# Optimization experiments

Hardware: AMD Instinct MI355X
Metric: run time of the kernel (lower is better)

## Reference

```python
import jax, jax.numpy as jnp
import numpy as np

NUM_USERS = 100000
NUM_ITEMS = 50000
EMB_DIM = 64
NUM_LAYERS = 3
N_EDGES = 3200000
BATCH = 16384


def setup_inputs() -> dict:
    key = jax.random.key(0)
    ks = jax.random.split(key, 6)
    user_emb = jax.random.normal(ks[0], (NUM_USERS, EMB_DIM), dtype=jnp.float32) * 0.1
    item_emb = jax.random.normal(ks[1], (NUM_ITEMS, EMB_DIM), dtype=jnp.float32) * 0.1
    # normalized adjacency values ~ 1/degree scale to keep propagation stable
    edge_vals = jax.random.uniform(ks[2], (N_EDGES,), dtype=jnp.float32) * (1.0 / 32.0)
    edge_u = jax.random.randint(ks[3], (N_EDGES,), 0, NUM_USERS, dtype=jnp.int32)
    edge_i = jax.random.randint(ks[4], (N_EDGES,), 0, NUM_ITEMS, dtype=jnp.int32)
    ku, ki = jax.random.split(ks[5])
    users = jax.random.randint(ku, (BATCH,), 0, NUM_USERS, dtype=jnp.int32)
    items = jax.random.randint(ki, (BATCH,), 0, NUM_ITEMS, dtype=jnp.int32)
    return {
        "user_emb": user_emb, "item_emb": item_emb, "edge_vals": edge_vals,
        "edge_u": edge_u, "edge_i": edge_i, "users": users, "items": items,
    }


def reference(user_emb, item_emb, edge_vals, edge_u, edge_i, users, items):
    num_users, num_items = user_emb.shape[0], item_emb.shape[0]
    e_u, e_i = user_emb, item_emb
    sum_u, sum_i = user_emb, item_emb
    for _ in range(NUM_LAYERS):
        # e_i^{k+1} = M_ui @ e_u^{k}  (SpMM: gather user rows, scatter-add to items)
        new_i = jax.ops.segment_sum(edge_vals[:, None] * e_u[edge_u], edge_i,
                                    num_segments=num_items)
        # e_u^{k+1} = M_iu @ e_i^{k}  (transpose SpMM)
        new_u = jax.ops.segment_sum(edge_vals[:, None] * e_i[edge_i], edge_u,
                                    num_segments=num_users)
        e_u, e_i = new_u, new_i
        sum_u = sum_u + e_u
        sum_i = sum_i + e_i
    inv = 1.0 / (NUM_LAYERS + 1)
    eu_f = sum_u * inv  # Eq (3.25): layer-mean
    ei_f = sum_i * inv
    # Eq (3.26): y_hat(u,i) = e_u^T e_i
    return (eu_f[users] * ei_f[items]).sum(axis=1)
```

## Files before the change

### kernel.cpp

```cpp
#include <hip/hip_runtime.h>
#include <stdint.h>

#define D 64
#define SH_I 8
#define SH_U 9
#define EPT 8
#define TILE 4096
#define PAD 8
#define SRT_CAP 18944

typedef unsigned long long u64;
typedef unsigned int u32;

#define DUMMY64 0xFFFFFFFF00000000ull


__device__ __forceinline__ u32 bf16_rne(float f) {
    u32 x = __float_as_uint(f);
    return (x + 0x7fffu + ((x >> 16) & 1u)) >> 16;
}
__device__ __forceinline__ u32 pack2_bf16(float a, float b) {
    return bf16_rne(a) | (bf16_rne(b) << 16);
}

__global__ __launch_bounds__(256)
void cvt_bf16_kernel(const float2* __restrict__ src, u32* __restrict__ dst, long n2) {
    long i = (long)blockIdx.x * blockDim.x + threadIdx.x;
    long stride = (long)gridDim.x * blockDim.x;
    for (; i < n2; i += stride) {
        float2 f = src[i];
        dst[i] = pack2_bf16(f.x, f.y);
    }
}


__device__ __forceinline__ int excl_scan_512t(int v, int* wsum) {
    int tid = threadIdx.x, lane = tid & 63, wid = tid >> 6;
    int x = v;
    #pragma unroll
    for (int d = 1; d < 64; d <<= 1) { int t = __shfl_up(x, d, 64); if (lane >= d) x += t; }
    if (lane == 63) wsum[wid] = x;
    __syncthreads();
    if (tid < 8) {
        int y = wsum[tid];
        #pragma unroll
        for (int d = 1; d < 8; d <<= 1) { int t = __shfl_up(y, d, 8); if (tid >= d) y += t; }
        wsum[tid] = y;
    }
    __syncthreads();
    return ((wid > 0) ? wsum[wid - 1] : 0) + x - v;
}

__device__ __forceinline__ int excl_scan_1024t(int v, int* wsum16) {
    int tid = threadIdx.x, lane = tid & 63, wid = tid >> 6;
    int x = v;
    #pragma unroll
    for (int d = 1; d < 64; d <<= 1) { int t = __shfl_up(x, d, 64); if (lane >= d) x += t; }
    if (lane == 63) wsum16[wid] = x;
    __syncthreads();
    if (tid < 16) {
        int y = wsum16[tid];
        #pragma unroll
        for (int d = 1; d < 16; d <<= 1) { int t = __shfl_up(y, d, 16); if (tid >= d) y += t; }
        wsum16[tid] = y;
    }
    __syncthreads();
    return ((wid > 0) ? wsum16[wid - 1] : 0) + x - v;
}


__global__ __launch_bounds__(512)
void init_cursors_kernel(int* cur_i, int* rc_i, int nb_i, int cap_i,
                         int* cur_u, int* rc_u, int nb_u, int cap_u) {
    int t = threadIdx.x;
    if (t < nb_i) { cur_i[t] = t * cap_i; rc_i[t] = 0; }
    if (t < nb_u) { cur_u[t] = t * cap_u; rc_u[t] = 0; }
}

__global__ __launch_bounds__(512)
void passA_kernel(const int* __restrict__ eu, const int* __restrict__ ei,
                  const float* __restrict__ ev, int E,
                  int* __restrict__ cur_i, int* __restrict__ rc_i,
                  int* __restrict__ cur_u, int* __restrict__ rc_u,
                  u64* __restrict__ stg_i, u64* __restrict__ stg_u) {
    __shared__ u64 stage[TILE];
    __shared__ int cnt[256], loffs[256], gbase[256];
    __shared__ int wsum[8];
    int tid = threadIdx.x;
    long tile0 = (long)blockIdx.x * TILE;
    int uu[EPT], ii[EPT], lo[EPT];
    u32 vv[EPT];
    #pragma unroll
    for (int j = 0; j < EPT; ++j) {
        long e = tile0 + tid + j * 512;
        if (e < E) {
            uu[j] = eu[e]; ii[j] = ei[e];
            vv[j] = bf16_rne(ev[e]) & 0x7fffu;
        } else {
            uu[j] = -1;
        }
    }

    if (tid < 256) cnt[tid] = 0;
    __syncthreads();
    #pragma unroll
    for (int j = 0; j < EPT; ++j)
        if (uu[j] >= 0) lo[j] = atomicAdd(&cnt[ii[j] >> SH_I], 1);
    __syncthreads();
    {
        int c = (tid < 256) ? cnt[tid] : 0;
        int excl = excl_scan_512t(c, wsum);
        if (tid < 256) {
            loffs[tid] = excl;
            if (c) {
                int cp = (c + PAD - 1) & ~(PAD - 1);
                gbase[tid] = atomicAdd(&cur_i[tid], cp);
                atomicAdd(&rc_i[tid], c);
            }
        }
    }
    __syncthreads();
    #pragma unroll
    for (int j = 0; j < EPT; ++j) {
        if (uu[j] >= 0) {
            int b = ii[j] >> SH_I;
            u32 rec = (vv[j] << 17) | (u32)uu[j];
            stage[loffs[b] + lo[j]] =
                ((u64)(u32)(ii[j] & ((1 << SH_I) - 1)) << 32) | rec;
        }
    }
    __syncthreads();
    {
        int w = tid >> 6, lane = tid & 63;
        for (int b = w; b < 256; b += 8) {
            int c = cnt[b];
            if (!c) continue;
            int cp = (c + PAD - 1) & ~(PAD - 1);
            int lb = loffs[b];
            long gb = gbase[b];
            for (int r = lane; r < cp; r += 64)
                stg_i[gb + r] = (r < c) ? stage[lb + r] : DUMMY64;
        }
    }
    __syncthreads();

    if (tid < 256) cnt[tid] = 0;
    __syncthreads();
    #pragma unroll
    for (int j = 0; j < EPT; ++j)
        if (uu[j] >= 0) lo[j] = atomicAdd(&cnt[uu[j] >> SH_U], 1);
    __syncthreads();
    {
        int c = (tid < 256) ? cnt[tid] : 0;
        int excl = excl_scan_512t(c, wsum);
        if (tid < 256) {
            loffs[tid] = excl;
            if (c) {
                int cp = (c + PAD - 1) & ~(PAD - 1);
                gbase[tid] = atomicAdd(&cur_u[tid], cp);
                atomicAdd(&rc_u[tid], c);
            }
        }
    }
    __syncthreads();
    #pragma unroll
    for (int j = 0; j < EPT; ++j) {
        if (uu[j] >= 0) {
            int b = uu[j] >> SH_U;
            u32 rec = (vv[j] << 17) | (u32)ii[j];
            stage[loffs[b] + lo[j]] =
                ((u64)(u32)(uu[j] & ((1 << SH_U) - 1)) << 32) | rec;
        }
    }
    __syncthreads();
    {
        int w = tid >> 6, lane = tid & 63;
        for (int b = w; b < 256; b += 8) {
            int c = cnt[b];
            if (!c) continue;
            int cp = (c + PAD - 1) & ~(PAD - 1);
            int lb = loffs[b];
            long gb = gbase[b];
            for (int r = lane; r < cp; r += 64)
                stg_u[gb + r] = (r < c) ? stage[lb + r] : DUMMY64;
        }
    }
}

__global__ __launch_bounds__(512)
void bucket_scan_kernel(const int* __restrict__ rc, int nb, int E,
                        int* __restrict__ bbase, int* __restrict__ rowp_sentinel) {
    __shared__ int wsum[8];
    int tid = threadIdx.x;
    int v = (tid < nb) ? rc[tid] : 0;
    int excl = excl_scan_512t(v, wsum);
    if (tid < nb) bbase[tid] = excl;
    if (tid == 0) *rowp_sentinel = E;
}

__global__ __launch_bounds__(1024)
void passB_kernel(int nb_i, int cap_i, int N_i,
                  int nb_u, int cap_u, int N_u,
                  const int* __restrict__ cur_i, const int* __restrict__ cur_u,
                  const int* __restrict__ rc_i, const int* __restrict__ rc_u,
                  const int* __restrict__ bb_i, const int* __restrict__ bb_u,
                  const u64* __restrict__ stg_i, const u64* __restrict__ stg_u,
                  int* __restrict__ rowp_i, int* __restrict__ rowp_u,
                  u32* __restrict__ csr_i, u32* __restrict__ csr_u) {
    __shared__ u32 srt[SRT_CAP];
    __shared__ int lcnt[512];
    __shared__ int wsum[16];
    int b = blockIdx.x;
    int dir_item = (b < nb_i);
    int bb = dir_item ? b : b - nb_i;
    int SH = dir_item ? SH_I : SH_U;
    int cap = dir_item ? cap_i : cap_u;
    int N = dir_item ? N_i : N_u;
    const u64* stg = dir_item ? stg_i : stg_u;
    int ebase = dir_item ? bb_i[bb] : bb_u[bb];
    int scount = (dir_item ? cur_i[bb] : cur_u[bb]) - bb * cap;
    int realcnt = dir_item ? rc_i[bb] : rc_u[bb];
    int* rowp = dir_item ? rowp_i : rowp_u;
    u32* csr = dir_item ? csr_i : csr_u;

    int rows0 = bb << SH;
    int nrows = min(1 << SH, N - rows0);
    int tid = threadIdx.x;
    const uint4* stg4 = (const uint4*)(stg + (size_t)bb * cap);
    int npair = scount >> 1;

    if (tid < 512) lcnt[tid] = 0;
    __syncthreads();
    for (int k = tid; k < npair; k += 1024) {
        uint4 w = stg4[k];
        if ((int)w.y >= 0) atomicAdd(&lcnt[(int)w.y], 1);
        if ((int)w.w >= 0) atomicAdd(&lcnt[(int)w.w], 1);
    }
    __syncthreads();
    int v = (tid < 512) ? lcnt[tid] : 0;
    int excl = excl_scan_1024t(v, wsum);
    if (tid < 512) lcnt[tid] = excl;
    if (tid < nrows) rowp[rows0 + tid] = ebase + excl;
    __syncthreads();
    for (int k = tid; k < npair; k += 1024) {
        uint4 w = stg4[k];
        if ((int)w.y >= 0) {
            int p = atomicAdd(&lcnt[(int)w.y], 1);
            if (p < SRT_CAP) srt[p] = w.x;
        }
        if ((int)w.w >= 0) {
            int p = atomicAdd(&lcnt[(int)w.w], 1);
            if (p < SRT_CAP) srt[p] = w.z;
        }
    }
    __syncthreads();
    int n = min(realcnt, SRT_CAP);
    for (int k = tid; k < n; k += 1024)
        csr[ebase + k] = srt[k];
}


template<int SAMPLED>
__global__ __launch_bounds__(256)
void spmm_kernel(const int* __restrict__ rowptr, const u32* __restrict__ csr,
                 const u32* __restrict__ src16, u32* __restrict__ dst16,
                 const int* __restrict__ idx, int nrows) {
    int slot = blockIdx.x * 4 + (threadIdx.x >> 6);
    if (slot >= nrows) return;
    int row = SAMPLED ? idx[slot] : slot;
    int lane = threadIdx.x & 63;
    int g = lane >> 4;
    int el = lane & 15;
    int beg = rowptr[row], end = rowptr[row + 1];
    const uint2* SB = (const uint2*)src16 + el;
    float4 A0 = {0,0,0,0}, A1 = {0,0,0,0}, A2 = {0,0,0,0}, A3 = {0,0,0,0};
    for (int k = beg + g; k < end; k += 16) {
        u32 r0 = csr[k];
        u32 r1 = csr[k + 4];
        u32 r2 = csr[k + 8];
        u32 r3 = csr[k + 12];
        bool m1 = (k + 4) < end, m2 = (k + 8) < end, m3 = (k + 12) < end;
        int s0 = (int)(r0 & 0x1ffffu);
        int s1 = m1 ? (int)(r1 & 0x1ffffu) : 0;
        int s2 = m2 ? (int)(r2 & 0x1ffffu) : 0;
        int s3 = m3 ? (int)(r3 & 0x1ffffu) : 0;
        float v0 = __uint_as_float((r0 & 0xfffe0000u) >> 1);
        float v1 = m1 ? __uint_as_float((r1 & 0xfffe0000u) >> 1) : 0.f;
        float v2 = m2 ? __uint_as_float((r2 & 0xfffe0000u) >> 1) : 0.f;
        float v3 = m3 ? __uint_as_float((r3 & 0xfffe0000u) >> 1) : 0.f;
        uint2 w0 = SB[(size_t)s0 * 16];
        uint2 w1 = SB[(size_t)s1 * 16];
        uint2 w2 = SB[(size_t)s2 * 16];
        uint2 w3 = SB[(size_t)s3 * 16];
        A0.x += v0 * __uint_as_float(w0.x << 16);
        A0.y += v0 * __uint_as_float(w0.x & 0xffff0000u);
        A0.z += v0 * __uint_as_float(w0.y << 16);
        A0.w += v0 * __uint_as_float(w0.y & 0xffff0000u);
        A1.x += v1 * __uint_as_float(w1.x << 16);
        A1.y += v1 * __uint_as_float(w1.x & 0xffff0000u);
        A1.z += v1 * __uint_as_float(w1.y << 16);
        A1.w += v1 * __uint_as_float(w1.y & 0xffff0000u);
        A2.x += v2 * __uint_as_float(w2.x << 16);
        A2.y += v2 * __uint_as_float(w2.x & 0xffff0000u);
        A2.z += v2 * __uint_as_float(w2.y << 16);
        A2.w += v2 * __uint_as_float(w2.y & 0xffff0000u);
        A3.x += v3 * __uint_as_float(w3.x << 16);
        A3.y += v3 * __uint_as_float(w3.x & 0xffff0000u);
        A3.z += v3 * __uint_as_float(w3.y << 16);
        A3.w += v3 * __uint_as_float(w3.y & 0xffff0000u);
    }
    float4 a;
    a.x = (A0.x + A1.x) + (A2.x + A3.x);
    a.y = (A0.y + A1.y) + (A2.y + A3.y);
    a.z = (A0.z + A1.z) + (A2.z + A3.z);
    a.w = (A0.w + A1.w) + (A2.w + A3.w);
    a.x += __shfl_xor(a.x, 16, 64); a.x += __shfl_xor(a.x, 32, 64);
    a.y += __shfl_xor(a.y, 16, 64); a.y += __shfl_xor(a.y, 32, 64);
    a.z += __shfl_xor(a.z, 16, 64); a.z += __shfl_xor(a.z, 32, 64);
    a.w += __shfl_xor(a.w, 16, 64); a.w += __shfl_xor(a.w, 32, 64);
    if (g == 0) {
        ((uint2*)dst16)[(size_t)slot * 16 + el] =
            make_uint2(pack2_bf16(a.x, a.y), pack2_bf16(a.z, a.w));
    }
}

__global__ __launch_bounds__(256)
void score_kernel(const float* __restrict__ user_emb, const float* __restrict__ item_emb,
                  const u32* __restrict__ eu1, const u32* __restrict__ eu2,
                  const u32* __restrict__ eu3s,
                  const u32* __restrict__ ei1, const u32* __restrict__ ei2,
                  const u32* __restrict__ ei3s,
                  const int* __restrict__ users, const int* __restrict__ items,
                  float* __restrict__ out, int B, float inv2) {
    int gid = blockIdx.x * blockDim.x + threadIdx.x;
    int b = gid >> 4;
    int lane = gid & 15;
    if (b >= B) return;
    int u = users[b], it = items[b];

    float4 su = ((const float4*)(user_emb + (size_t)u * D))[lane];
    uint2 p1 = ((const uint2*)eu1)[(size_t)u * 16 + lane];
    uint2 p2 = ((const uint2*)eu2)[(size_t)u * 16 + lane];
    uint2 p3 = ((const uint2*)eu3s)[(size_t)b * 16 + lane];
    su.x += __uint_as_float(p1.x << 16) + __uint_as_float(p2.x << 16) + __uint_as_float(p3.x << 16);
    su.y += __uint_as_float(p1.x & 0xffff0000u) + __uint_as_float(p2.x & 0xffff0000u) + __uint_as_float(p3.x & 0xffff0000u);
    su.z += __uint_as_float(p1.y << 16) + __uint_as_float(p2.y << 16) + __uint_as_float(p3.y << 16);
    su.w += __uint_as_float(p1.y & 0xffff0000u) + __uint_as_float(p2.y & 0xffff0000u) + __uint_as_float(p3.y & 0xffff0000u);

    float4 si = ((const float4*)(item_emb + (size_t)it * D))[lane];
    uint2 q1 = ((const uint2*)ei1)[(size_t)it * 16 + lane];
    uint2 q2 = ((const uint2*)ei2)[(size_t)it * 16 + lane];
    uint2 q3 = ((const uint2*)ei3s)[(size_t)b * 16 + lane];
    si.x += __uint_as_float(q1.x << 16) + __uint_as_float(q2.x << 16) + __uint_as_float(q3.x << 16);
    si.y += __uint_as_float(q1.x & 0xffff0000u) + __uint_as_float(q2.x & 0xffff0000u) + __uint_as_float(q3.x & 0xffff0000u);
    si.z += __uint_as_float(q1.y << 16) + __uint_as_float(q2.y << 16) + __uint_as_float(q3.y << 16);
    si.w += __uint_as_float(q1.y & 0xffff0000u) + __uint_as_float(q2.y & 0xffff0000u) + __uint_as_float(q3.y & 0xffff0000u);

    float d = su.x * si.x + su.y * si.y + su.z * si.z + su.w * si.w;
    #pragma unroll
    for (int m = 1; m < 16; m <<= 1) d += __shfl_xor(d, m, 64);
    if (lane == 0) out[b] = d * inv2;
}


extern "C" void kernel_launch(void* const* d_in, const int* in_sizes, int n_in,
                              void* d_out, int out_size, void* d_ws, size_t ws_size,
                              hipStream_t stream) {
    const float* user_emb = (const float*)d_in[0];
    const float* item_emb = (const float*)d_in[1];
    const float* edge_vals = (const float*)d_in[2];
    const int* edge_u = (const int*)d_in[3];
    const int* edge_i = (const int*)d_in[4];
    const int* users = (const int*)d_in[5];
    const int* items = (const int*)d_in[6];
    float* out = (float*)d_out;

    const int U = in_sizes[0] / D;
    const int I = in_sizes[1] / D;
    const int E = in_sizes[2];
    const int B = in_sizes[5];

    const int nb_i = (I + (1 << SH_I) - 1) >> SH_I;
    const int nb_u = (U + (1 << SH_U) - 1) >> SH_U;
    const int tiles = (E + TILE - 1) / TILE;
    const int cap_i = ((E / nb_i + tiles * (PAD - 1) + 1024 + 63) / 64) * 64;
    const int cap_u = ((E / nb_u + tiles * (PAD - 1) + 1024 + 63) / 64) * 64;

    char* p = (char*)d_ws;
    size_t off = 0;
    auto alloc = [&](size_t bytes) -> char* {
        char* r = p + off;
        off = (off + bytes + 255) & ~(size_t)255;
        return r;
    };
    u32* ub16  = (u32*)alloc((size_t)U * (D / 2) * 4);
    u32* ib16  = (u32*)alloc((size_t)I * (D / 2) * 4);
    u32* eu1   = (u32*)alloc((size_t)U * (D / 2) * 4);
    u32* eu2   = (u32*)alloc((size_t)U * (D / 2) * 4);
    u32* ei1   = (u32*)alloc((size_t)I * (D / 2) * 4);
    u32* ei2   = (u32*)alloc((size_t)I * (D / 2) * 4);
    u32* eu3s  = (u32*)alloc((size_t)B * (D / 2) * 4);
    u32* ei3s  = (u32*)alloc((size_t)B * (D / 2) * 4);
    u32* csr_u = (u32*)alloc((size_t)(E + 16) * 4);
    u32* csr_i = (u32*)alloc((size_t)(E + 16) * 4);
    int* rowp_u = (int*)alloc((size_t)(U + 1) * 4);
    int* rowp_i = (int*)alloc((size_t)(I + 1) * 4);
    int* cur_i  = (int*)alloc((size_t)nb_i * 4);
    int* cur_u  = (int*)alloc((size_t)nb_u * 4);
    int* rc_i   = (int*)alloc((size_t)nb_i * 4);
    int* rc_u   = (int*)alloc((size_t)nb_u * 4);
    int* bb_i   = (int*)alloc((size_t)nb_i * 4);
    int* bb_u   = (int*)alloc((size_t)nb_u * 4);
    u64* stg_i  = (u64*)alloc((size_t)nb_i * cap_i * 8);
    u64* stg_u  = (u64*)alloc((size_t)nb_u * cap_u * 8);
    if (off > ws_size) return;

    cvt_bf16_kernel<<<1024, 256, 0, stream>>>((const float2*)user_emb, ub16, (long)U * (D / 2));
    cvt_bf16_kernel<<<1024, 256, 0, stream>>>((const float2*)item_emb, ib16, (long)I * (D / 2));

    init_cursors_kernel<<<1, 512, 0, stream>>>(cur_i, rc_i, nb_i, cap_i,
                                               cur_u, rc_u, nb_u, cap_u);
    passA_kernel<<<tiles, 512, 0, stream>>>(edge_u, edge_i, edge_vals, E,
                                            cur_i, rc_i, cur_u, rc_u,
                                            stg_i, stg_u);
    bucket_scan_kernel<<<1, 512, 0, stream>>>(rc_i, nb_i, E, bb_i, rowp_i + I);
    bucket_scan_kernel<<<1, 512, 0, stream>>>(rc_u, nb_u, E, bb_u, rowp_u + U);
    passB_kernel<<<nb_i + nb_u, 1024, 0, stream>>>(nb_i, cap_i, I, nb_u, cap_u, U,
                                                   cur_i, cur_u, rc_i, rc_u,
                                                   bb_i, bb_u,
                                                   stg_i, stg_u, rowp_i, rowp_u,
                                                   csr_i, csr_u);

    int blk_i = (I + 3) / 4;
    int blk_u = (U + 3) / 4;
    int blk_s = (B + 3) / 4;
    spmm_kernel<0><<<blk_i, 256, 0, stream>>>(rowp_i, csr_i, ub16, ei1, nullptr, I);
    spmm_kernel<0><<<blk_u, 256, 0, stream>>>(rowp_u, csr_u, ib16, eu1, nullptr, U);
    spmm_kernel<0><<<blk_i, 256, 0, stream>>>(rowp_i, csr_i, eu1, ei2, nullptr, I);
    spmm_kernel<0><<<blk_u, 256, 0, stream>>>(rowp_u, csr_u, ei1, eu2, nullptr, U);
    spmm_kernel<1><<<blk_s, 256, 0, stream>>>(rowp_i, csr_i, eu2, ei3s, items, B);
    spmm_kernel<1><<<blk_s, 256, 0, stream>>>(rowp_u, csr_u, ei2, eu3s, users, B);

    int blk_sc = (B * 16 + 255) / 256;
    score_kernel<<<blk_sc, 256, 0, stream>>>(user_emb, item_emb,
                                             eu1, eu2, eu3s, ei1, ei2, ei3s,
                                             users, items, out, B, 0.0625f);
}
```

Measured before the change: 321.7 us.

## Split bf16 embeddings into two column planes and run SpMM per half

```diff
diff --git a/kernel.cpp b/kernel.cpp
--- a/kernel.cpp
+++ b/kernel.cpp
@@ -24,12 +24,15 @@
 }
 
 __global__ __launch_bounds__(256)
-void cvt_bf16_kernel(const float2* __restrict__ src, u32* __restrict__ dst, long n2) {
+void cvt_bf16_kernel(const float2* __restrict__ src, u32* __restrict__ dst, int N) {
+    long n = (long)N * 32;
     long i = (long)blockIdx.x * blockDim.x + threadIdx.x;
     long stride = (long)gridDim.x * blockDim.x;
-    for (; i < n2; i += stride) {
+    for (; i < n; i += stride) {
         float2 f = src[i];
-        dst[i] = pack2_bf16(f.x, f.y);
+        long row = i >> 5;
+        int c = (int)(i & 31);
+        dst[(size_t)(c >> 4) * N * 16 + row * 16 + (c & 15)] = pack2_bf16(f.x, f.y);
     }
 }
 
@@ -132,13 +135,14 @@
     __syncthreads();
     {
         int w = tid >> 6, lane = tid & 63;
-        for (int b = w; b < 256; b += 8) {
+        int sub = lane >> 4, l16 = lane & 15;
+        for (int b = w * 4 + sub; b < 256; b += 32) {
             int c = cnt[b];
             if (!c) continue;
             int cp = (c + PAD - 1) & ~(PAD - 1);
             int lb = loffs[b];
             long gb = gbase[b];
-            for (int r = lane; r < cp; r += 64)
+            for (int r = l16; r < cp; r += 16)
                 stg_i[gb + r] = (r < c) ? stage[lb + r] : DUMMY64;
         }
     }
@@ -175,13 +179,14 @@
     __syncthreads();
     {
         int w = tid >> 6, lane = tid & 63;
-        for (int b = w; b < 256; b += 8) {
+        int sub = lane >> 4, l16 = lane & 15;
+        for (int b = w * 4 + sub; b < 256; b += 32) {
             int c = cnt[b];
             if (!c) continue;
             int cp = (c + PAD - 1) & ~(PAD - 1);
             int lb = loffs[b];
             long gb = gbase[b];
-            for (int r = lane; r < cp; r += 64)
+            for (int r = l16; r < cp; r += 16)
                 stg_u[gb + r] = (r < c) ? stage[lb + r] : DUMMY64;
         }
     }
@@ -260,19 +265,66 @@
 }
 
 
-template<int SAMPLED>
 __global__ __launch_bounds__(256)
-void spmm_kernel(const int* __restrict__ rowptr, const u32* __restrict__ csr,
-                 const u32* __restrict__ src16, u32* __restrict__ dst16,
-                 const int* __restrict__ idx, int nrows) {
+void spmm_half_kernel(const int* __restrict__ rowptr, const u32* __restrict__ csr,
+                      const u32* __restrict__ srcp, u32* __restrict__ dstp,
+                      int nrows) {
+    int row = blockIdx.x * 4 + (threadIdx.x >> 6);
+    if (row >= nrows) return;
+    int lane = threadIdx.x & 63;
+    int g = lane >> 3;
+    int el = lane & 7;
+    int beg = rowptr[row], end = rowptr[row + 1];
+    const uint2* SB = (const uint2*)srcp + el;
+    float4 A0 = {0,0,0,0}, A1 = {0,0,0,0};
+    for (int k = beg + g; k < end; k += 16) {
+        u32 r0 = __builtin_nontemporal_load(csr + k);
+        u32 r1 = __builtin_nontemporal_load(csr + k + 8);
+        bool m1 = (k + 8) < end;
+        int s0 = (int)(r0 & 0x1ffffu);
+        int s1 = m1 ? (int)(r1 & 0x1ffffu) : 0;
+        float v0 = __uint_as_float((r0 & 0xfffe0000u) >> 1);
+        float v1 = m1 ? __uint_as_float((r1 & 0xfffe0000u) >> 1) : 0.f;
+        uint2 w0 = SB[(size_t)s0 * 8];
+        uint2 w1 = SB[(size_t)s1 * 8];
+        A0.x += v0 * __uint_as_float(w0.x << 16);
+        A0.y += v0 * __uint_as_float(w0.x & 0xffff0000u);
+        A0.z += v0 * __uint_as_float(w0.y << 16);
+        A0.w += v0 * __uint_as_float(w0.y & 0xffff0000u);
+        A1.x += v1 * __uint_as_float(w1.x << 16);
+        A1.y += v1 * __uint_as_float(w1.x & 0xffff0000u);
+        A1.z += v1 * __uint_as_float(w1.y << 16);
+        A1.w += v1 * __uint_as_float(w1.y & 0xffff0000u);
+    }
+    float4 a;
+    a.x = A0.x + A1.x; a.y = A0.y + A1.y; a.z = A0.z + A1.z; a.w = A0.w + A1.w;
+    #pragma unroll
+    for (int m = 8; m < 64; m <<= 1) {
+        a.x += __shfl_xor(a.x, m, 64);
+        a.y += __shfl_xor(a.y, m, 64);
+        a.z += __shfl_xor(a.z, m, 64);
+        a.w += __shfl_xor(a.w, m, 64);
+    }
+    if (g == 0) {
+        u64 o = (u64)pack2_bf16(a.x, a.y) | ((u64)pack2_bf16(a.z, a.w) << 32);
+        __builtin_nontemporal_store(o, (u64*)dstp + (size_t)row * 8 + el);
+    }
+}
+
+__global__ __launch_bounds__(256)
+void spmm_sampled_kernel(const int* __restrict__ rowptr, const u32* __restrict__ csr,
+                         const u32* __restrict__ src_base, int splaneN,
+                         u32* __restrict__ dst16, const int* __restrict__ idx,
+                         int nrows) {
     int slot = blockIdx.x * 4 + (threadIdx.x >> 6);
     if (slot >= nrows) return;
-    int row = SAMPLED ? idx[slot] : slot;
+    int row = idx[slot];
     int lane = threadIdx.x & 63;
     int g = lane >> 4;
     int el = lane & 15;
     int beg = rowptr[row], end = rowptr[row + 1];
-    const uint2* SB = (const uint2*)src16 + el;
+    const uint2* SB = (const uint2*)(src_base + (size_t)(el >> 3) * splaneN * 16)
+                      + (el & 7);
     float4 A0 = {0,0,0,0}, A1 = {0,0,0,0}, A2 = {0,0,0,0}, A3 = {0,0,0,0};
     for (int k = beg + g; k < end; k += 16) {
         u32 r0 = csr[k];
@@ -288,10 +340,10 @@
         float v1 = m1 ? __uint_as_float((r1 & 0xfffe0000u) >> 1) : 0.f;
         float v2 = m2 ? __uint_as_float((r2 & 0xfffe0000u) >> 1) : 0.f;
         float v3 = m3 ? __uint_as_float((r3 & 0xfffe0000u) >> 1) : 0.f;
-        uint2 w0 = SB[(size_t)s0 * 16];
-        uint2 w1 = SB[(size_t)s1 * 16];
-        uint2 w2 = SB[(size_t)s2 * 16];
-        uint2 w3 = SB[(size_t)s3 * 16];
+        uint2 w0 = SB[(size_t)s0 * 8];
+        uint2 w1 = SB[(size_t)s1 * 8];
+        uint2 w2 = SB[(size_t)s2 * 8];
+        uint2 w3 = SB[(size_t)s3 * 8];
         A0.x += v0 * __uint_as_float(w0.x << 16);
         A0.y += v0 * __uint_as_float(w0.x & 0xffff0000u);
         A0.z += v0 * __uint_as_float(w0.y << 16);
@@ -331,16 +383,19 @@
                   const u32* __restrict__ ei1, const u32* __restrict__ ei2,
                   const u32* __restrict__ ei3s,
                   const int* __restrict__ users, const int* __restrict__ items,
-                  float* __restrict__ out, int B, float inv2) {
+                  float* __restrict__ out, int B, int U, int I, float inv2) {
     int gid = blockIdx.x * blockDim.x + threadIdx.x;
     int b = gid >> 4;
     int lane = gid & 15;
     if (b >= B) return;
     int u = users[b], it = items[b];
+    size_t upoff = (size_t)(lane >> 3) * U * 16;
+    size_t ipoff = (size_t)(lane >> 3) * I * 16;
+    int col = lane & 7;
 
     float4 su = ((const float4*)(user_emb + (size_t)u * D))[lane];
-    uint2 p1 = ((const uint2*)eu1)[(size_t)u * 16 + lane];
-    uint2 p2 = ((const uint2*)eu2)[(size_t)u * 16 + lane];
+    uint2 p1 = ((const uint2*)(eu1 + upoff))[(size_t)u * 8 + col];
+    uint2 p2 = ((const uint2*)(eu2 + upoff))[(size_t)u * 8 + col];
     uint2 p3 = ((const uint2*)eu3s)[(size_t)b * 16 + lane];
     su.x += __uint_as_float(p1.x << 16) + __uint_as_float(p2.x << 16) + __uint_as_float(p3.x << 16);
     su.y += __uint_as_float(p1.x & 0xffff0000u) + __uint_as_float(p2.x & 0xffff0000u) + __uint_as_float(p3.x & 0xffff0000u);
@@ -348,8 +403,8 @@
     su.w += __uint_as_float(p1.y & 0xffff0000u) + __uint_as_float(p2.y & 0xffff0000u) + __uint_as_float(p3.y & 0xffff0000u);
 
     float4 si = ((const float4*)(item_emb + (size_t)it * D))[lane];
-    uint2 q1 = ((const uint2*)ei1)[(size_t)it * 16 + lane];
-    uint2 q2 = ((const uint2*)ei2)[(size_t)it * 16 + lane];
+    uint2 q1 = ((const uint2*)(ei1 + ipoff))[(size_t)it * 8 + col];
+    uint2 q2 = ((const uint2*)(ei2 + ipoff))[(size_t)it * 8 + col];
     uint2 q3 = ((const uint2*)ei3s)[(size_t)b * 16 + lane];
     si.x += __uint_as_float(q1.x << 16) + __uint_as_float(q2.x << 16) + __uint_as_float(q3.x << 16);
     si.y += __uint_as_float(q1.x & 0xffff0000u) + __uint_as_float(q2.x & 0xffff0000u) + __uint_as_float(q3.x & 0xffff0000u);
@@ -415,8 +470,8 @@
     u64* stg_u  = (u64*)alloc((size_t)nb_u * cap_u * 8);
     if (off > ws_size) return;
 
-    cvt_bf16_kernel<<<1024, 256, 0, stream>>>((const float2*)user_emb, ub16, (long)U * (D / 2));
-    cvt_bf16_kernel<<<1024, 256, 0, stream>>>((const float2*)item_emb, ib16, (long)I * (D / 2));
+    cvt_bf16_kernel<<<1024, 256, 0, stream>>>((const float2*)user_emb, ub16, U);
+    cvt_bf16_kernel<<<1024, 256, 0, stream>>>((const float2*)item_emb, ib16, I);
 
     init_cursors_kernel<<<1, 512, 0, stream>>>(cur_i, rc_i, nb_i, cap_i,
                                                cur_u, rc_u, nb_u, cap_u);
@@ -434,15 +489,20 @@
     int blk_i = (I + 3) / 4;
     int blk_u = (U + 3) / 4;
     int blk_s = (B + 3) / 4;
-    spmm_kernel<0><<<blk_i, 256, 0, stream>>>(rowp_i, csr_i, ub16, ei1, nullptr, I);
-    spmm_kernel<0><<<blk_u, 256, 0, stream>>>(rowp_u, csr_u, ib16, eu1, nullptr, U);
-    spmm_kernel<0><<<blk_i, 256, 0, stream>>>(rowp_i, csr_i, eu1, ei2, nullptr, I);
-    spmm_kernel<0><<<blk_u, 256, 0, stream>>>(rowp_u, csr_u, ei1, eu2, nullptr, U);
-    spmm_kernel<1><<<blk_s, 256, 0, stream>>>(rowp_i, csr_i, eu2, ei3s, items, B);
-    spmm_kernel<1><<<blk_s, 256, 0, stream>>>(rowp_u, csr_u, ei2, eu3s, users, B);
+    const size_t UP = (size_t)U * 16, IP = (size_t)I * 16;
+    spmm_half_kernel<<<blk_i, 256, 0, stream>>>(rowp_i, csr_i, ub16,      ei1,      I);
+    spmm_half_kernel<<<blk_i, 256, 0, stream>>>(rowp_i, csr_i, ub16 + UP, ei1 + IP, I);
+    spmm_half_kernel<<<blk_u, 256, 0, stream>>>(rowp_u, csr_u, ib16,      eu1,      U);
+    spmm_half_kernel<<<blk_u, 256, 0, stream>>>(rowp_u, csr_u, ib16 + IP, eu1 + UP, U);
+    spmm_half_kernel<<<blk_i, 256, 0, stream>>>(rowp_i, csr_i, eu1,      ei2,      I);
+    spmm_half_kernel<<<blk_i, 256, 0, stream>>>(rowp_i, csr_i, eu1 + UP, ei2 + IP, I);
+    spmm_half_kernel<<<blk_u, 256, 0, stream>>>(rowp_u, csr_u, ei1,      eu2,      U);
+    spmm_half_kernel<<<blk_u, 256, 0, stream>>>(rowp_u, csr_u, ei1 + IP, eu2 + UP, U);
+    spmm_sampled_kernel<<<blk_s, 256, 0, stream>>>(rowp_i, csr_i, eu2, U, ei3s, items, B);
+    spmm_sampled_kernel<<<blk_s, 256, 0, stream>>>(rowp_u, csr_u, ei2, I, eu3s, users, B);
 
     int blk_sc = (B * 16 + 255) / 256;
     score_kernel<<<blk_sc, 256, 0, stream>>>(user_emb, item_emb,
                                              eu1, eu2, eu3s, ei1, ei2, ei3s,
-                                             users, items, out, B, 0.0625f);
-}
+                                             users, items, out, B, U, I, 0.0625f);
+}
```

Result: slower. 497.2 us (+54.6%).

## Widen SpMM gathers to 16-byte loads and split bucket flush into quarter-waves

Applied to the files above, without the earlier changes.

```diff
diff --git a/kernel.cpp b/kernel.cpp
--- a/kernel.cpp
+++ b/kernel.cpp
@@ -22,6 +22,8 @@
 __device__ __forceinline__ u32 pack2_bf16(float a, float b) {
     return bf16_rne(a) | (bf16_rne(b) << 16);
 }
+__device__ __forceinline__ float blo(u32 w) { return __uint_as_float(w << 16); }
+__device__ __forceinline__ float bhi(u32 w) { return __uint_as_float(w & 0xffff0000u); }
 
 __global__ __launch_bounds__(256)
 void cvt_bf16_kernel(const float2* __restrict__ src, u32* __restrict__ dst, long n2) {
@@ -132,13 +134,14 @@
     __syncthreads();
     {
         int w = tid >> 6, lane = tid & 63;
-        for (int b = w; b < 256; b += 8) {
+        int sub = lane >> 4, l16 = lane & 15;
+        for (int b = w * 4 + sub; b < 256; b += 32) {
             int c = cnt[b];
             if (!c) continue;
             int cp = (c + PAD - 1) & ~(PAD - 1);
             int lb = loffs[b];
             long gb = gbase[b];
-            for (int r = lane; r < cp; r += 64)
+            for (int r = l16; r < cp; r += 16)
                 stg_i[gb + r] = (r < c) ? stage[lb + r] : DUMMY64;
         }
     }
@@ -175,13 +178,14 @@
     __syncthreads();
     {
         int w = tid >> 6, lane = tid & 63;
-        for (int b = w; b < 256; b += 8) {
+        int sub = lane >> 4, l16 = lane & 15;
+        for (int b = w * 4 + sub; b < 256; b += 32) {
             int c = cnt[b];
             if (!c) continue;
             int cp = (c + PAD - 1) & ~(PAD - 1);
             int lb = loffs[b];
             long gb = gbase[b];
-            for (int r = lane; r < cp; r += 64)
+            for (int r = l16; r < cp; r += 16)
                 stg_u[gb + r] = (r < c) ? stage[lb + r] : DUMMY64;
         }
     }
@@ -269,58 +273,45 @@
     if (slot >= nrows) return;
     int row = SAMPLED ? idx[slot] : slot;
     int lane = threadIdx.x & 63;
-    int g = lane >> 4;
-    int el = lane & 15;
+    int g = lane >> 3;
+    int el = lane & 7;
     int beg = rowptr[row], end = rowptr[row + 1];
-    const uint2* SB = (const uint2*)src16 + el;
-    float4 A0 = {0,0,0,0}, A1 = {0,0,0,0}, A2 = {0,0,0,0}, A3 = {0,0,0,0};
+    const uint4* SB = (const uint4*)src16 + el;
+    float A0[8] = {0,0,0,0,0,0,0,0}, A1[8] = {0,0,0,0,0,0,0,0};
     for (int k = beg + g; k < end; k += 16) {
         u32 r0 = csr[k];
-        u32 r1 = csr[k + 4];
-        u32 r2 = csr[k + 8];
-        u32 r3 = csr[k + 12];
-        bool m1 = (k + 4) < end, m2 = (k + 8) < end, m3 = (k + 12) < end;
+        u32 r1 = csr[k + 8];
+        bool m1 = (k + 8) < end;
         int s0 = (int)(r0 & 0x1ffffu);
         int s1 = m1 ? (int)(r1 & 0x1ffffu) : 0;
-        int s2 = m2 ? (int)(r2 & 0x1ffffu) : 0;
-        int s3 = m3 ? (int)(r3 & 0x1ffffu) : 0;
         float v0 = __uint_as_float((r0 & 0xfffe0000u) >> 1);
         float v1 = m1 ? __uint_as_float((r1 & 0xfffe0000u) >> 1) : 0.f;
-        float v2 = m2 ? __uint_as_float((r2 & 0xfffe0000u) >> 1) : 0.f;
-        float v3 = m3 ? __uint_as_float((r3 & 0xfffe0000u) >> 1) : 0.f;
-        uint2 w0 = SB[(size_t)s0 * 16];
-        uint2 w1 = SB[(size_t)s1 * 16];
-        uint2 w2 = SB[(size_t)s2 * 16];
-        uint2 w3 = SB[(size_t)s3 * 16];
-        A0.x += v0 * __uint_as_float(w0.x << 16);
-        A0.y += v0 * __uint_as_float(w0.x & 0xffff0000u);
-        A0.z += v0 * __uint_as_float(w0.y << 16);
-        A0.w += v0 * __uint_as_float(w0.y & 0xffff0000u);
-        A1.x += v1 * __uint_as_float(w1.x << 16);
-        A1.y += v1 * __uint_as_float(w1.x & 0xffff0000u);
-        A1.z += v1 * __uint_as_float(w1.y << 16);
-        A1.w += v1 * __uint_as_float(w1.y & 0xffff0000u);
-        A2.x += v2 * __uint_as_float(w2.x << 16);
-        A2.y += v2 * __uint_as_float(w2.x & 0xffff0000u);
-        A2.z += v2 * __uint_as_float(w2.y << 16);
-        A2.w += v2 * __uint_as_float(w2.y & 0xffff0000u);
-        A3.x += v3 * __uint_as_float(w3.x << 16);
-        A3.y += v3 * __uint_as_float(w3.x & 0xffff0000u);
-        A3.z += v3 * __uint_as_float(w3.y << 16);
-        A3.w += v3 * __uint_as_float(w3.y & 0xffff0000u);
-    }
-    float4 a;
-    a.x = (A0.x + A1.x) + (A2.x + A3.x);
-    a.y = (A0.y + A1.y) + (A2.y + A3.y);
-    a.z = (A0.z + A1.z) + (A2.z + A3.z);
-    a.w = (A0.w + A1.w) + (A2.w + A3.w);
-    a.x += __shfl_xor(a.x, 16, 64); a.x += __shfl_xor(a.x, 32, 64);
-    a.y += __shfl_xor(a.y, 16, 64); a.y += __shfl_xor(a.y, 32, 64);
-    a.z += __shfl_xor(a.z, 16, 64); a.z += __shfl_xor(a.z, 32, 64);
-    a.w += __shfl_xor(a.w, 16, 64); a.w += __shfl_xor(a.w, 32, 64);
+        uint4 w0 = SB[(size_t)s0 * 8];
+        uint4 w1 = SB[(size_t)s1 * 8];
+        A0[0] += v0 * blo(w0.x); A0[1] += v0 * bhi(w0.x);
+        A0[2] += v0 * blo(w0.y); A0[3] += v0 * bhi(w0.y);
+        A0[4] += v0 * blo(w0.z); A0[5] += v0 * bhi(w0.z);
+        A0[6] += v0 * blo(w0.w); A0[7] += v0 * bhi(w0.w);
+        A1[0] += v1 * blo(w1.x); A1[1] += v1 * bhi(w1.x);
+        A1[2] += v1 * blo(w1.y); A1[3] += v1 * bhi(w1.y);
+        A1[4] += v1 * blo(w1.z); A1[5] += v1 * bhi(w1.z);
+        A1[6] += v1 * blo(w1.w); A1[7] += v1 * bhi(w1.w);
+    }
+    float a[8];
+    #pragma unroll
+    for (int j = 0; j < 8; ++j) a[j] = A0[j] + A1[j];
+    #pragma unroll
+    for (int m = 8; m < 64; m <<= 1) {
+        #pragma unroll
+        for (int j = 0; j < 8; ++j) a[j] += __shfl_xor(a[j], m, 64);
+    }
     if (g == 0) {
-        ((uint2*)dst16)[(size_t)slot * 16 + el] =
-            make_uint2(pack2_bf16(a.x, a.y), pack2_bf16(a.z, a.w));
+        uint4 o;
+        o.x = pack2_bf16(a[0], a[1]);
+        o.y = pack2_bf16(a[2], a[3]);
+        o.z = pack2_bf16(a[4], a[5]);
+        o.w = pack2_bf16(a[6], a[7]);
+        ((uint4*)dst16)[(size_t)slot * 8 + el] = o;
     }
 }
 
@@ -342,19 +333,19 @@
     uint2 p1 = ((const uint2*)eu1)[(size_t)u * 16 + lane];
     uint2 p2 = ((const uint2*)eu2)[(size_t)u * 16 + lane];
     uint2 p3 = ((const uint2*)eu3s)[(size_t)b * 16 + lane];
-    su.x += __uint_as_float(p1.x << 16) + __uint_as_float(p2.x << 16) + __uint_as_float(p3.x << 16);
-    su.y += __uint_as_float(p1.x & 0xffff0000u) + __uint_as_float(p2.x & 0xffff0000u) + __uint_as_float(p3.x & 0xffff0000u);
-    su.z += __uint_as_float(p1.y << 16) + __uint_as_float(p2.y << 16) + __uint_as_float(p3.y << 16);
-    su.w += __uint_as_float(p1.y & 0xffff0000u) + __uint_as_float(p2.y & 0xffff0000u) + __uint_as_float(p3.y & 0xffff0000u);
+    su.x += blo(p1.x) + blo(p2.x) + blo(p3.x);
+    su.y += bhi(p1.x) + bhi(p2.x) + bhi(p3.x);
+    su.z += blo(p1.y) + blo(p2.y) + blo(p3.y);
+    su.w += bhi(p1.y) + bhi(p2.y) + bhi(p3.y);
 
     float4 si = ((const float4*)(item_emb + (size_t)it * D))[lane];
     uint2 q1 = ((const uint2*)ei1)[(size_t)it * 16 + lane];
     uint2 q2 = ((const uint2*)ei2)[(size_t)it * 16 + lane];
     uint2 q3 = ((const uint2*)ei3s)[(size_t)b * 16 + lane];
-    si.x += __uint_as_float(q1.x << 16) + __uint_as_float(q2.x << 16) + __uint_as_float(q3.x << 16);
-    si.y += __uint_as_float(q1.x & 0xffff0000u) + __uint_as_float(q2.x & 0xffff0000u) + __uint_as_float(q3.x & 0xffff0000u);
-    si.z += __uint_as_float(q1.y << 16) + __uint_as_float(q2.y << 16) + __uint_as_float(q3.y << 16);
-    si.w += __uint_as_float(q1.y & 0xffff0000u) + __uint_as_float(q2.y & 0xffff0000u) + __uint_as_float(q3.y & 0xffff0000u);
+    si.x += blo(q1.x) + blo(q2.x) + blo(q3.x);
+    si.y += bhi(q1.x) + bhi(q2.x) + bhi(q3.x);
+    si.z += blo(q1.y) + blo(q2.y) + blo(q3.y);
+    si.w += bhi(q1.y) + bhi(q2.y) + bhi(q3.y);
 
     float d = su.x * si.x + su.y * si.y + su.z * si.z + su.w * si.w;
     #pragma unroll
```

After: 311.2 us. 1.03x faster.
